# Optimization experiments

Hardware: AMD Instinct MI355X
Metric: run time of the kernel (lower is better)

## Reference

```python
import jax, jax.numpy as jnp
import numpy as np

B_, L_, D_MODEL, N_LAYER, VOCAB = 4, 2048, 512, 2, 128
D_INNER, D_STATE, DT_RANK, D_CONV = 2 * D_MODEL, 16, D_MODEL // 16, 4
NDIR = 2  # forward / backward Mamba stacks


def setup_inputs() -> dict:
    key = jax.random.key(0)
    ks = jax.random.split(key, 12)
    f = jax.random.normal
    A_init = jnp.broadcast_to(
        jnp.log(jnp.arange(1, D_STATE + 1, dtype=jnp.float32)),
        (NDIR, N_LAYER, D_INNER, D_STATE)) + 0.0
    return {
        "input_ids": jax.random.randint(ks[0], (B_, L_), 0, VOCAB),
        "padding_mask": jnp.ones((B_, L_), dtype=bool),
        "embed": 0.02 * f(ks[1], (NDIR, VOCAB, D_MODEL)),
        "in_proj_w": 0.02 * f(ks[2], (NDIR, N_LAYER, 2 * D_INNER, D_MODEL)),
        "conv_w": 0.1 * f(ks[3], (NDIR, N_LAYER, D_INNER, 1, D_CONV)),
        "conv_b": 0.1 * f(ks[4], (NDIR, N_LAYER, D_INNER)),
        "x_proj_w": 0.02 * f(ks[5], (NDIR, N_LAYER, DT_RANK + 2 * D_STATE, D_INNER)),
        "dt_proj_w": 0.1 * f(ks[6], (NDIR, N_LAYER, D_INNER, DT_RANK)),
        "dt_proj_b": -4.0 + 0.5 * jax.random.uniform(ks[7], (NDIR, N_LAYER, D_INNER)),
        "A_log": A_init,
        "D": jnp.ones((NDIR, N_LAYER, D_INNER)),
        "out_proj_w": 0.02 * f(ks[8], (NDIR, N_LAYER, D_MODEL, D_INNER)),
        "norm_w": jnp.ones((NDIR, N_LAYER, D_MODEL)),
        "norm_f_w": jnp.ones((NDIR, D_MODEL)),
        "proj_w": 0.02 * f(ks[9], (D_MODEL, 2 * D_MODEL)),
        "proj_b": jnp.zeros((D_MODEL,)),
    }


def _rmsnorm(x, w, eps=1e-5):
    return x * jax.lax.rsqrt(jnp.mean(jnp.square(x), axis=-1, keepdims=True) + eps) * w


def _selective_scan(u, dt, Bm, Cm, A, Dp):
    # u, dt: (b, l, d_inner); Bm, Cm: (b, l, d_state)
    b, l, di = u.shape

    def step(h, inp):
        u_t, dt_t, b_t, c_t = inp                      # (b,di) (b,di) (b,n) (b,n)
        dA = jnp.exp(dt_t[:, :, None] * A)             # (b, di, n)
        h = dA * h + (dt_t * u_t)[:, :, None] * b_t[:, None, :]
        return h, jnp.einsum('bdn,bn->bd', h, c_t)

    h0 = jnp.zeros((b, di, A.shape[-1]), u.dtype)
    xs = (jnp.swapaxes(u, 0, 1), jnp.swapaxes(dt, 0, 1),
          jnp.swapaxes(Bm, 0, 1), jnp.swapaxes(Cm, 0, 1))
    _, ys = jax.lax.scan(step, h0, xs)                 # ys: (l, b, di)
    return jnp.swapaxes(ys, 0, 1) + u * Dp


def _mamba(x, p):
    in_w, cw, cb, xw, dtw, dtb, alog, dp, ow = p
    xz = jnp.einsum('bld,ed->ble', x, in_w)            # (b, l, 2*d_inner)
    u, z = jnp.split(xz, 2, axis=-1)
    uc = jnp.swapaxes(u, 1, 2)                         # (b, d_inner, l)
    uc = jax.lax.conv_general_dilated(
        uc, cw, (1,), [(D_CONV - 1, 0)], feature_group_count=D_INNER)
    u = jax.nn.silu(jnp.swapaxes(uc + cb[None, :, None], 1, 2))
    xdbl = jnp.einsum('bld,ed->ble', u, xw)
    dt, Bm, Cm = jnp.split(xdbl, [DT_RANK, DT_RANK + D_STATE], axis=-1)
    dt = jax.nn.softplus(jnp.einsum('blr,dr->bld', dt, dtw) + dtb)
    y = _selective_scan(u, dt, Bm, Cm, -jnp.exp(alog), dp)
    y = y * jax.nn.silu(z)
    return jnp.einsum('bld,ed->ble', y, ow)


def _mixer(ids, d, embed, in_proj_w, conv_w, conv_b, x_proj_w, dt_proj_w,
           dt_proj_b, A_log, D, out_proj_w, norm_w, norm_f_w):
    hidden = embed[d][ids]
    residual = None
    for i in range(N_LAYER):
        residual = hidden if residual is None else hidden + residual
        hidden = _rmsnorm(residual, norm_w[d, i])
        p = (in_proj_w[d, i], conv_w[d, i], conv_b[d, i], x_proj_w[d, i],
             dt_proj_w[d, i], dt_proj_b[d, i], A_log[d, i], D[d, i],
             out_proj_w[d, i])
        hidden = _mamba(hidden, p)
    return _rmsnorm(hidden + residual, norm_f_w[d])


def reference(input_ids, padding_mask, embed, in_proj_w, conv_w, conv_b,
              x_proj_w, dt_proj_w, dt_proj_b, A_log, D, out_proj_w, norm_w,
              norm_f_w, proj_w, proj_b):
    args = (embed, in_proj_w, conv_w, conv_b, x_proj_w, dt_proj_w, dt_proj_b,
            A_log, D, out_proj_w, norm_w, norm_f_w)
    fwd = _mixer(input_ids, 0, *args)
    bwd = jnp.flip(_mixer(jnp.flip(input_ids, 1), 1, *args), 1)
    out = jnp.concatenate([fwd, bwd], axis=-1)        # (b, l, 2*d_model)
    return jnp.einsum('ble,oe->blo', out, proj_w) + proj_b
```

## Files before the change

kernel.cpp:

```cpp
#include <hip/hip_runtime.h>
#include <hip/hip_bf16.h>

#define B_   4
#define L_   2048
#define DM   512
#define DI   1024
#define NST  16
#define DTR  32
#define ROWS (B_ * L_)
#define NCHUNK 64
#define CLEN  (L_ / NCHUNK)
#define LN2R 1.4426950408889634f

typedef unsigned short u16;
typedef __attribute__((ext_vector_type(8))) short bf16x8;
typedef __attribute__((ext_vector_type(4))) float f32x4;
typedef __attribute__((ext_vector_type(4))) float float4v;
typedef __attribute__((ext_vector_type(2))) float f32x2;

__device__ __forceinline__ float bf2f(u16 h) {
  union { unsigned int u; float f; } v; v.u = ((unsigned int)h) << 16; return v.f;
}
__device__ __forceinline__ u16 f2bf(float f) {
  union { float f; unsigned int u; } v; v.f = f;
  unsigned int u = v.u;
  if ((u & 0x7fffffffu) > 0x7f800000u) return (u16)((u >> 16) | 0x0040u);
  return (u16)((u + 0x7fffu + ((u >> 16) & 1u)) >> 16);
}
__device__ __forceinline__ float sigmoidf_(float x) { return 1.f / (1.f + __expf(-x)); }

__device__ __forceinline__ f32x2 pk_mul(f32x2 a, f32x2 b) {
  f32x2 d; asm("v_pk_mul_f32 %0, %1, %2" : "=v"(d) : "v"(a), "v"(b)); return d;
}
__device__ __forceinline__ f32x2 pk_fma(f32x2 a, f32x2 b, f32x2 c) {
  f32x2 d; asm("v_pk_fma_f32 %0, %1, %2, %3" : "=v"(d) : "v"(a), "v"(b), "v"(c)); return d;
}

__device__ __forceinline__ void gload16(const u16* g, u16* l) {
  __builtin_amdgcn_global_load_lds(
      (const __attribute__((address_space(1))) void*)g,
      (__attribute__((address_space(3))) void*)l, 16, 0, 0);
}

__global__ __launch_bounds__(256) void cvt_k(const float* __restrict__ in,
                                             u16* __restrict__ out, int n4) {
  int i = blockIdx.x * 256 + threadIdx.x;
  if (i >= n4) return;
  float4v v = *(const float4v*)&in[i * 4];
  u16 o[4];
  o[0] = f2bf(v.x); o[1] = f2bf(v.y); o[2] = f2bf(v.z); o[3] = f2bf(v.w);
  *(ulong1*)&out[i * 4] = *(ulong1*)o;
}

__global__ __launch_bounds__(256) void trp_k(const float* __restrict__ in,
                                             float* __restrict__ out) {
  int o = blockIdx.x * 256 + threadIdx.x;
  int li = o >> 15;
  int k = (o >> 10) & (DTR - 1);
  int d = o & (DI - 1);
  out[o] = in[((size_t)li * DI + d) * DTR + k];
}

__global__ __launch_bounds__(256) void embed_k(const int* __restrict__ ids,
                                               const float* __restrict__ emb,
                                               float* __restrict__ res, int flip) {
  int idx = blockIdx.x * 256 + threadIdx.x;
  int c = idx & (DM - 1);
  int row = idx >> 9;
  int b = row >> 11;
  int l = row & (L_ - 1);
  int sl = flip ? (L_ - 1 - l) : l;
  int id = ids[(b << 11) + sl];
  res[idx] = emb[id * DM + c];
}

template <bool ADD>
__global__ __launch_bounds__(256) void addnorm_k(float* __restrict__ res,
                                                 const float* __restrict__ hid,
                                                 const float* __restrict__ w,
                                                 u16* __restrict__ xn) {
  int row = blockIdx.x;
  int tid = threadIdx.x;
  int base = row * DM;
  float x0 = res[base + tid];
  float x1 = res[base + 256 + tid];
  if (ADD) {
    x0 += hid[base + tid];
    x1 += hid[base + 256 + tid];
    res[base + tid] = x0;
    res[base + 256 + tid] = x1;
  }
  float s = x0 * x0 + x1 * x1;
  for (int off = 32; off; off >>= 1) s += __shfl_xor(s, off);
  __shared__ float ps[4];
  if (!(tid & 63)) ps[tid >> 6] = s;
  __syncthreads();
  float tot = ps[0] + ps[1] + ps[2] + ps[3];
  float rs = 1.f / sqrtf(tot / (float)DM + 1e-5f);
  xn[base + tid]       = f2bf(x0 * rs * w[tid]);
  xn[base + 256 + tid] = f2bf(x1 * rs * w[tid + 256]);
}

#define MFMA_B16(a, b, c) __builtin_amdgcn_mfma_f32_16x16x32_bf16(a, b, c, 0, 0, 0)

__global__ __launch_bounds__(512) void gemm8p_k(const u16* __restrict__ A,
                                                const u16* __restrict__ W,
                                                u16* __restrict__ outp,
                                                int N, int K) {
  __shared__ u16 As[2][2][256 * 32];
  __shared__ u16 Wsh[2][2][256 * 32];
  int tid = threadIdx.x;
  int lane = tid & 63;
  int wv = tid >> 6;
  int wr = wv >> 2, wc = wv & 3;
  int bid = blockIdx.x;
  int xcd = bid & 7, jj = bid >> 3;
  int mt = (xcd & 3) * 8 + (jj & 7);
  int nt = (xcd >> 2) * 4 + (jj >> 3);
  int m0 = mt * 256, n0 = nt * 256;
  f32x4 acc[8][4];
#pragma unroll
  for (int i = 0; i < 8; ++i)
#pragma unroll
    for (int j = 0; j < 4; ++j) acc[i][j] = (f32x4){0.f, 0.f, 0.f, 0.f};
  int rr = lane & 15;
  int sl = lane >> 4;
  int pofs = ((sl + (rr >> 1)) & 3) * 8;
  int lr = lane >> 2;
  int ls = ((lane & 3) - (lr >> 1)) & 3;

  auto stA = [&](int tau, int ks) {
    int buf = tau & 1;
#pragma unroll
    for (int j = 0; j < 2; ++j)
      gload16(A + (size_t)(m0 + j * 128 + wv * 16 + lr) * K + tau * 64 + ks * 32 + ls * 8,
              &As[buf][ks][(j * 128 + wv * 16) * 32]);
  };
  auto stW = [&](int tau, int ks) {
    int buf = tau & 1;
#pragma unroll
    for (int j = 0; j < 2; ++j)
      gload16(W + (size_t)(n0 + j * 128 + wv * 16 + lr) * K + tau * 64 + ks * 32 + ls * 8,
              &Wsh[buf][ks][(j * 128 + wv * 16) * 32]);
  };

  int NT = K / 64;
  stA(0, 0); stW(0, 0); stA(0, 1); stW(0, 1);
  asm volatile("s_waitcnt vmcnt(4)" ::: "memory");
  __builtin_amdgcn_sched_barrier(0);
  __builtin_amdgcn_s_barrier();
  __builtin_amdgcn_sched_barrier(0);

  for (int tau = 0; tau < NT; ++tau) {
    int buf = tau & 1;
    bool more = (tau + 1 < NT);
    bf16x8 af[8], w0, w1;
#pragma unroll
    for (int mi = 0; mi < 8; ++mi)
      af[mi] = *(bf16x8*)&As[buf][0][(wr * 128 + mi * 16 + rr) * 32 + pofs];
    w0 = *(bf16x8*)&Wsh[buf][0][(wc * 64 + 0 * 16 + rr) * 32 + pofs];
    w1 = *(bf16x8*)&Wsh[buf][0][(wc * 64 + 1 * 16 + rr) * 32 + pofs];
    if (more) stA(tau + 1, 0);
    __builtin_amdgcn_sched_barrier(0);
    __builtin_amdgcn_s_barrier();
    asm volatile("s_waitcnt lgkmcnt(0)" ::: "memory");
    __builtin_amdgcn_sched_barrier(0);
    __builtin_amdgcn_s_setprio(1);
#pragma unroll
    for (int mi = 0; mi < 8; ++mi) {
      acc[mi][0] = MFMA_B16(af[mi], w0, acc[mi][0]);
      acc[mi][1] = MFMA_B16(af[mi], w1, acc[mi][1]);
    }
    __builtin_amdgcn_s_setprio(0);
    __builtin_amdgcn_s_barrier();
    __builtin_amdgcn_sched_barrier(0);
    w0 = *(bf16x8*)&Wsh[buf][0][(wc * 64 + 2 * 16 + rr) * 32 + pofs];
    w1 = *(bf16x8*)&Wsh[buf][0][(wc * 64 + 3 * 16 + rr) * 32 + pofs];
    if (more) {
      stW(tau + 1, 0);
      asm volatile("s_waitcnt vmcnt(4)" ::: "memory");
    } else {
      asm volatile("s_waitcnt vmcnt(0)" ::: "memory");
    }
    __builtin_amdgcn_sched_barrier(0);
    __builtin_amdgcn_s_barrier();
    asm volatile("s_waitcnt lgkmcnt(0)" ::: "memory");
    __builtin_amdgcn_sched_barrier(0);
    __builtin_amdgcn_s_setprio(1);
#pragma unroll
    for (int mi = 0; mi < 8; ++mi) {
      acc[mi][2] = MFMA_B16(af[mi], w0, acc[mi][2]);
      acc[mi][3] = MFMA_B16(af[mi], w1, acc[mi][3]);
    }
    __builtin_amdgcn_s_setprio(0);
    __builtin_amdgcn_s_barrier();
    __builtin_amdgcn_sched_barrier(0);
#pragma unroll
    for (int mi = 0; mi < 8; ++mi)
      af[mi] = *(bf16x8*)&As[buf][1][(wr * 128 + mi * 16 + rr) * 32 + pofs];
    w0 = *(bf16x8*)&Wsh[buf][1][(wc * 64 + 0 * 16 + rr) * 32 + pofs];
    w1 = *(bf16x8*)&Wsh[buf][1][(wc * 64 + 1 * 16 + rr) * 32 + pofs];
    if (more) stA(tau + 1, 1);
    __builtin_amdgcn_sched_barrier(0);
    __builtin_amdgcn_s_barrier();
    asm volatile("s_waitcnt lgkmcnt(0)" ::: "memory");
    __builtin_amdgcn_sched_barrier(0);
    __builtin_amdgcn_s_setprio(1);
#pragma unroll
    for (int mi = 0; mi < 8; ++mi) {
      acc[mi][0] = MFMA_B16(af[mi], w0, acc[mi][0]);
      acc[mi][1] = MFMA_B16(af[mi], w1, acc[mi][1]);
    }
    __builtin_amdgcn_s_setprio(0);
    __builtin_amdgcn_s_barrier();
    __builtin_amdgcn_sched_barrier(0);
    w0 = *(bf16x8*)&Wsh[buf][1][(wc * 64 + 2 * 16 + rr) * 32 + pofs];
    w1 = *(bf16x8*)&Wsh[buf][1][(wc * 64 + 3 * 16 + rr) * 32 + pofs];
    if (more) {
      stW(tau + 1, 1);
      asm volatile("s_waitcnt vmcnt(4)" ::: "memory");
    }
    __builtin_amdgcn_sched_barrier(0);
    __builtin_amdgcn_s_barrier();
    asm volatile("s_waitcnt lgkmcnt(0)" ::: "memory");
    __builtin_amdgcn_sched_barrier(0);
    __builtin_amdgcn_s_setprio(1);
#pragma unroll
    for (int mi = 0; mi < 8; ++mi) {
      acc[mi][2] = MFMA_B16(af[mi], w0, acc[mi][2]);
      acc[mi][3] = MFMA_B16(af[mi], w1, acc[mi][3]);
    }
    __builtin_amdgcn_s_setprio(0);
    __builtin_amdgcn_s_barrier();
    __builtin_amdgcn_sched_barrier(0);
  }
  int cr = (lane >> 4) << 2;
  int cc = lane & 15;
#pragma unroll
  for (int mi = 0; mi < 8; ++mi)
#pragma unroll
    for (int ni = 0; ni < 4; ++ni) {
      int row = m0 + wr * 128 + mi * 16 + cr;
      int col = n0 + wc * 64 + ni * 16 + cc;
#pragma unroll
      for (int j = 0; j < 4; ++j)
        outp[(size_t)(row + j) * N + col] = f2bf(acc[mi][ni][j]);
    }
}

#define EPI_F32  0
#define EPI_BF16 1
#define EPI_BIAS 2

template <int BN, int EPI, int SK = 1>
__global__ __launch_bounds__(256) void gemm_bt(const u16* __restrict__ A,
                                               const u16* __restrict__ W,
                                               void* __restrict__ outp,
                                               const float* __restrict__ bias,
                                               int N, int K) {
  constexpr int BM = 128, BK = 32;
  constexpr int NF = BN / 32;
  constexpr int G = (BN == 128) ? 4 : 3;
  __shared__ u16 As[4][BM * BK];
  __shared__ u16 Wsh[4][BN * BK];
  int tid = threadIdx.x;
  int lane = tid & 63;
  int wv = tid >> 6;
  int wr = wv >> 1, wc = wv & 1;
  int m0 = blockIdx.x * BM;
  int n0 = (SK > 1) ? 0 : blockIdx.y * BN;
  int koff = (SK > 1) ? blockIdx.y * (K / SK) : 0;
  int KS = K / SK;
  int NK = KS / BK;
  f32x4 acc[4][NF];
#pragma unroll
  for (int i = 0; i < 4; ++i)
#pragma unroll
    for (int j = 0; j < NF; ++j) acc[i][j] = (f32x4){0.f, 0.f, 0.f, 0.f};
  int rr = lane & 15;
  int kk = (lane >> 4) << 3;
  int l4 = lane >> 2;
  int c8 = (lane & 3) << 3;
  const u16* Ag = A + (size_t)(m0 + l4) * K + koff + c8;
  const u16* Wg = W + (size_t)(n0 + l4) * K + koff + c8;

  auto stage = [&](int k0, int buf) {
    gload16(Ag + (size_t)(wv * 16) * K + k0, &As[buf][wv * 512]);
    gload16(Ag + (size_t)((wv + 4) * 16) * K + k0, &As[buf][(wv + 4) * 512]);
    gload16(Wg + (size_t)(wv * 16) * K + k0, &Wsh[buf][wv * 512]);
    if (BN == 128)
      gload16(Wg + (size_t)((wv + 4) * 16) * K + k0, &Wsh[buf][(wv + 4) * 512]);
  };

  stage(0, 0); stage(BK, 1); stage(2 * BK, 2);
  for (int k = 0; k < NK; ++k) {
    if (k < NK - 2)
      asm volatile("s_waitcnt vmcnt(%0)" :: "n"(2 * G) : "memory");
    else if (k == NK - 2)
      asm volatile("s_waitcnt vmcnt(%0)" :: "n"(G) : "memory");
    else
      asm volatile("s_waitcnt vmcnt(0)" ::: "memory");
    __builtin_amdgcn_s_barrier();
    __builtin_amdgcn_sched_barrier(0);
    if (k + 3 < NK) stage((k + 3) * BK, (k + 3) & 3);
    __builtin_amdgcn_sched_barrier(0);
    int cur = k & 3;
    bf16x8 af[4], wf[NF];
#pragma unroll
    for (int mi = 0; mi < 4; ++mi)
      af[mi] = *(bf16x8*)&As[cur][(wr * 64 + mi * 16 + rr) * BK + kk];
#pragma unroll
    for (int ni = 0; ni < NF; ++ni)
      wf[ni] = *(bf16x8*)&Wsh[cur][(wc * (BN / 2) + ni * 16 + rr) * BK + kk];
#pragma unroll
    for (int mi = 0; mi < 4; ++mi)
#pragma unroll
      for (int ni = 0; ni < NF; ++ni)
        acc[mi][ni] = __builtin_amdgcn_mfma_f32_16x16x32_bf16(af[mi], wf[ni], acc[mi][ni], 0, 0, 0);
  }
  int cr = (lane >> 4) << 2;
  int cc = lane & 15;
  float* outF = (float*)outp + ((SK > 1) ? (size_t)blockIdx.y * (size_t)ROWS * N : 0);
#pragma unroll
  for (int mi = 0; mi < 4; ++mi)
#pragma unroll
    for (int ni = 0; ni < NF; ++ni) {
      int row = m0 + wr * 64 + mi * 16 + cr;
      int col = n0 + wc * (BN / 2) + ni * 16 + cc;
      float bv = (EPI == EPI_BIAS) ? bias[col] : 0.f;
#pragma unroll
      for (int j = 0; j < 4; ++j) {
        float v = acc[mi][ni][j] + bv;
        if (EPI == EPI_BF16)
          ((u16*)outp)[(size_t)(row + j) * N + col] = f2bf(v);
        else
          outF[(size_t)(row + j) * N + col] = v;
      }
    }
}

__global__ __launch_bounds__(256) void conv_k(const u16* __restrict__ xz,
                                              const float* __restrict__ cw,
                                              const float* __restrict__ cb,
                                              u16* __restrict__ uh) {
  int idx = blockIdx.x * 256 + threadIdx.x;
  int c = idx & (DI - 1);
  int row = idx >> 10;
  int l = row & (L_ - 1);
  float acc = cb[c];
#pragma unroll
  for (int j = 0; j < 4; ++j) {
    int ls = l + j - 3;
    if (ls >= 0)
      acc += bf2f(xz[(size_t)(row + j - 3) * (2 * DI) + c]) * cw[c * 4 + j];
  }
  float s = acc * sigmoidf_(acc);
  uh[idx] = f2bf(s);
}

__device__ __forceinline__ bool a_fast(const float* alog, int d, float& a20) {
  a20 = -__expf(alog[d * NST]) * LN2R;
  bool fast = true;
#pragma unroll
  for (int n = 1; n < NST; ++n) {
    float an = -__expf(alog[d * NST + n]) * LN2R;
    fast &= (fabsf(an - (float)(n + 1) * a20) <= 1e-5f * (float)(n + 1) * fabsf(a20));
  }
  return fast;
}

__device__ __forceinline__ void stage_xs(float (*xs)[64], const float* xp,
                                         int b, int t0, int tid) {
  size_t base = ((size_t)b * L_ + t0) * 64;
  const float4v* s0 = (const float4v*)(xp + base);
  const float4v* s1 = (const float4v*)(xp + (size_t)ROWS * 64 + base);
  const float4v* s2 = (const float4v*)(xp + (size_t)2 * ROWS * 64 + base);
  const float4v* s3 = (const float4v*)(xp + (size_t)3 * ROWS * 64 + base);
  float4v* dst = (float4v*)&xs[0][0];
  dst[tid]       = s0[tid]       + s1[tid]       + s2[tid]       + s3[tid];
  dst[tid + 256] = s0[tid + 256] + s1[tid + 256] + s2[tid + 256] + s3[tid + 256];
}

__global__ __launch_bounds__(256) void dtscan1_k(const u16* __restrict__ uh,
                                                 const float* __restrict__ xp,
                                                 const float* __restrict__ dtw_t,
                                                 const float* __restrict__ dtb,
                                                 const float* __restrict__ alog,
                                                 float* __restrict__ dtf,
                                                 float* __restrict__ chk) {
  __shared__ float xs[CLEN][64];
  int blk = blockIdx.x;
  int db = blk & 3;
  int c  = (blk >> 2) & (NCHUNK - 1);
  int b  = blk >> 8;
  int tid = threadIdx.x;
  int d  = db * 256 + tid;
  int t0 = c * CLEN;
  stage_xs(xs, xp, b, t0, tid);
  f32x2 w2[16];
#pragma unroll
  for (int j = 0; j < 16; ++j)
    w2[j] = (f32x2){dtw_t[(size_t)(2 * j) * DI + d], dtw_t[(size_t)(2 * j + 1) * DI + d]};
  float bias = dtb[d];
  float a20;
  bool fast = a_fast(alog, d, a20);
  __syncthreads();
  float S = 0.f;
  size_t ubase = ((size_t)b * L_ + t0) * DI + d;
  f32x2 h2[8];
#pragma unroll
  for (int q = 0; q < 8; ++q) h2[q] = (f32x2){0.f, 0.f};
  for (int t = 0; t < CLEN; ++t) {
    f32x2 a2 = {bias, 0.f};
    const f32x2* xr2 = (const f32x2*)&xs[t][0];
#pragma unroll
    for (int j = 0; j < 16; ++j) a2 = pk_fma(xr2[j], w2[j], a2);
    float a = a2.x + a2.y;
    float dtv = (a > 15.f) ? a : __logf(1.f + __expf(a));
    dtf[ubase] = dtv;
    float du = dtv * bf2f(uh[ubase]);
    S += dtv;
    if (fast) {
      float p1 = exp2f(dtv * a20);
      float p2 = p1 * p1;
      f32x2 pw = {p1, p2};
      f32x2 pst = {p2, p2};
      f32x2 du2 = {du, du};
#pragma unroll
      for (int k = 0; k < 4; ++k) {
        f32x4 bv = *(const f32x4*)&xs[t][DTR + k * 4];
        f32x2 blo = __builtin_shufflevector(bv, bv, 0, 1);
        f32x2 bhi = __builtin_shufflevector(bv, bv, 2, 3);
        h2[2 * k]     = pk_fma(pw, h2[2 * k], pk_mul(du2, blo));
        pw = pk_mul(pw, pst);
        h2[2 * k + 1] = pk_fma(pw, h2[2 * k + 1], pk_mul(du2, bhi));
        if (k < 3) pw = pk_mul(pw, pst);
      }
    } else {
#pragma unroll
      for (int q = 0; q < 8; ++q) {
        float e0 = exp2f(dtv * -__expf(alog[d * NST + 2 * q]) * LN2R);
        float e1 = exp2f(dtv * -__expf(alog[d * NST + 2 * q + 1]) * LN2R);
        f32x2 bv = *(const f32x2*)&xs[t][DTR + q * 2];
        h2[q] = pk_fma((f32x2){e0, e1}, h2[q], pk_mul((f32x2){du, du}, bv));
      }
    }
    ubase += DI;
  }
  const size_t H = (size_t)B_ * NCHUNK * DI * NST;
  size_t idx = ((size_t)(b * NCHUNK + c) * DI + d) * NST;
#pragma unroll
  for (int n = 0; n < NST; ++n) {
    float an = -__expf(alog[d * NST + n]) * LN2R;
    chk[idx + n]     = exp2f(an * S);
    chk[H + idx + n] = (n & 1) ? h2[n >> 1].y : h2[n >> 1].x;
  }
}

__global__ __launch_bounds__(256) void scan2_k(float* __restrict__ chk) {
  int j = blockIdx.x * 256 + threadIdx.x;
  int n = j & 15;
  int d = (j >> 4) & (DI - 1);
  int b = j >> 14;
  const size_t H = (size_t)B_ * NCHUNK * DI * NST;
  float h = 0.f;
  for (int c = 0; c < NCHUNK; ++c) {
    size_t idx = ((size_t)(b * NCHUNK + c) * DI + d) * NST + n;
    float a = chk[idx];
    float hl = chk[H + idx];
    chk[H + idx] = h;
    h = a * h + hl;
  }
}

__global__ __launch_bounds__(256) void scan3_k(const u16* __restrict__ uh,
                                               const float* __restrict__ dtf,
                                               const float* __restrict__ xp,
                                               const float* __restrict__ alog,
                                               const float* __restrict__ dvec,
                                               const float* __restrict__ chk,
                                               const u16* __restrict__ xz,
                                               u16* __restrict__ yg) {
  __shared__ float xs[CLEN][64];
  int blk = blockIdx.x;
  int db = blk & 3;
  int c  = (blk >> 2) & (NCHUNK - 1);
  int b  = blk >> 8;
  int tid = threadIdx.x;
  int d  = db * 256 + tid;
  int t0 = c * CLEN;
  stage_xs(xs, xp, b, t0, tid);
  float a20;
  bool fast = a_fast(alog, d, a20);
  const size_t H = (size_t)B_ * NCHUNK * DI * NST;
  size_t cidx = ((size_t)(b * NCHUNK + c) * DI + d) * NST;
  f32x2 h2[8];
#pragma unroll
  for (int q = 0; q < 8; ++q) h2[q] = *(const f32x2*)&chk[H + cidx + 2 * q];
  float Dv = dvec[d];
  __syncthreads();
  size_t ubase = ((size_t)b * L_ + t0) * DI + d;
  size_t zbase = ((size_t)b * L_ + t0) * (2 * DI) + DI + d;
  if (fast) {
    for (int t = 0; t < CLEN; ++t) {
      float dtv = dtf[ubase];
      float uv  = bf2f(uh[ubase]);
      float du  = dtv * uv;
      float p1 = exp2f(dtv * a20);
      float p2 = p1 * p1;
      f32x2 pw = {p1, p2};
      f32x2 pst = {p2, p2};
      f32x2 du2 = {du, du};
      f32x2 acc2 = {0.f, 0.f};
#pragma unroll
      for (int k = 0; k < 4; ++k) {
        f32x4 bv = *(const f32x4*)&xs[t][DTR + k * 4];
        f32x4 cv = *(const f32x4*)&xs[t][DTR + NST + k * 4];
        f32x2 blo = __builtin_shufflevector(bv, bv, 0, 1);
        f32x2 bhi = __builtin_shufflevector(bv, bv, 2, 3);
        f32x2 clo = __builtin_shufflevector(cv, cv, 0, 1);
        f32x2 chi = __builtin_shufflevector(cv, cv, 2, 3);
        h2[2 * k]     = pk_fma(pw, h2[2 * k], pk_mul(du2, blo));
        acc2          = pk_fma(h2[2 * k], clo, acc2);
        pw = pk_mul(pw, pst);
        h2[2 * k + 1] = pk_fma(pw, h2[2 * k + 1], pk_mul(du2, bhi));
        acc2          = pk_fma(h2[2 * k + 1], chi, acc2);
        if (k < 3) pw = pk_mul(pw, pst);
      }
      float y = acc2.x + acc2.y + uv * Dv;
      float z = bf2f(xz[zbase]);
      yg[ubase] = f2bf(y * z * sigmoidf_(z));
      ubase += DI; zbase += 2 * DI;
    }
  } else {
    float A2[NST];
#pragma unroll
    for (int n = 0; n < NST; ++n) A2[n] = -__expf(alog[d * NST + n]) * LN2R;
    for (int t = 0; t < CLEN; ++t) {
      float dtv = dtf[ubase];
      float uv  = bf2f(uh[ubase]);
      float du  = dtv * uv;
      f32x2 acc2 = {0.f, 0.f};
#pragma unroll
      for (int q = 0; q < 8; ++q) {
        f32x2 bv = *(const f32x2*)&xs[t][DTR + q * 2];
        f32x2 cv = *(const f32x2*)&xs[t][DTR + NST + q * 2];
        f32x2 e = {exp2f(dtv * A2[2 * q]), exp2f(dtv * A2[2 * q + 1])};
        h2[q] = pk_fma(e, h2[q], pk_mul((f32x2){du, du}, bv));
        acc2 = pk_fma(h2[q], cv, acc2);
      }
      float y = acc2.x + acc2.y + uv * Dv;
      float z = bf2f(xz[zbase]);
      yg[ubase] = f2bf(y * z * sigmoidf_(z));
      ubase += DI; zbase += 2 * DI;
    }
  }
}

__global__ __launch_bounds__(256) void fincat_k(const float* __restrict__ hid,
                                                const float* __restrict__ res,
                                                const float* __restrict__ w,
                                                u16* __restrict__ cat, int dir) {
  int row = blockIdx.x;
  int tid = threadIdx.x;
  int base = row * DM;
  float x0 = hid[base + tid] + res[base + tid];
  float x1 = hid[base + 256 + tid] + res[base + 256 + tid];
  float s = x0 * x0 + x1 * x1;
  for (int off = 32; off; off >>= 1) s += __shfl_xor(s, off);
  __shared__ float ps[4];
  if (!(tid & 63)) ps[tid >> 6] = s;
  __syncthreads();
  float tot = ps[0] + ps[1] + ps[2] + ps[3];
  float rs = 1.f / sqrtf(tot / (float)DM + 1e-5f);
  int b = row >> 11, l = row & (L_ - 1);
  size_t drow = dir ? ((size_t)(b << 11) + (L_ - 1 - l)) : (size_t)row;
  size_t obase = drow * (2 * DM) + (size_t)dir * DM;
  cat[obase + tid]       = f2bf(x0 * rs * w[tid]);
  cat[obase + 256 + tid] = f2bf(x1 * rs * w[tid + 256]);
}

extern "C" void kernel_launch(void* const* d_in, const int* in_sizes, int n_in,
                              void* d_out, int out_size, void* d_ws, size_t ws_size,
                              hipStream_t stream) {
  const int*   ids      = (const int*)d_in[0];
  const float* embed    = (const float*)d_in[2];
  const float* in_w     = (const float*)d_in[3];
  const float* conv_w   = (const float*)d_in[4];
  const float* conv_b   = (const float*)d_in[5];
  const float* x_w      = (const float*)d_in[6];
  const float* dt_w     = (const float*)d_in[7];
  const float* dt_bias  = (const float*)d_in[8];
  const float* A_log    = (const float*)d_in[9];
  const float* Dp       = (const float*)d_in[10];
  const float* out_w    = (const float*)d_in[11];
  const float* norm_w   = (const float*)d_in[12];
  const float* norm_f   = (const float*)d_in[13];
  const float* proj_w   = (const float*)d_in[14];
  const float* proj_b   = (const float*)d_in[15];

  char* ws = (char*)d_ws;
  size_t off = 0;
  auto alloc = [&](size_t bytes) {
    void* p = ws + off;
    off += (bytes + 255) & ~(size_t)255;
    return p;
  };
  float* res  = (float*)alloc((size_t)ROWS * DM * 4);
  float* hid  = (float*)alloc((size_t)ROWS * DM * 4);
  u16*   xnyg = (u16*)alloc((size_t)ROWS * DI * 2);
  u16*   xz   = (u16*)alloc((size_t)ROWS * 2 * DI * 2);
  u16*   u_h  = (u16*)alloc((size_t)ROWS * DI * 2);
  float* dtf  = (float*)alloc((size_t)ROWS * DI * 4);
  float* chk  = (float*)alloc((size_t)2 * B_ * NCHUNK * DI * NST * 4);
  u16*   cat  = (u16*)alloc((size_t)ROWS * 2 * DM * 2);
  const int N_IN  = 4 * 2 * DI * DM;
  const int N_XW  = 4 * 64 * DI;
  const int N_OW  = 4 * DM * DI;
  const int N_PW  = DM * 2 * DM;
  const int N_DTW = 4 * DTR * DI;
  u16*   in_wb  = (u16*)alloc((size_t)N_IN * 2);
  u16*   x_wb   = (u16*)alloc((size_t)N_XW * 2);
  u16*   out_wb = (u16*)alloc((size_t)N_OW * 2);
  u16*   pr_wb  = (u16*)alloc((size_t)N_PW * 2);
  float* dtw_t  = (float*)alloc((size_t)N_DTW * 4);
  if (off > ws_size) return;

  cvt_k<<<(N_IN / 4 + 255) / 256, 256, 0, stream>>>(in_w, in_wb, N_IN / 4);
  cvt_k<<<(N_XW / 4 + 255) / 256, 256, 0, stream>>>(x_w, x_wb, N_XW / 4);
  cvt_k<<<(N_OW / 4 + 255) / 256, 256, 0, stream>>>(out_w, out_wb, N_OW / 4);
  cvt_k<<<(N_PW / 4 + 255) / 256, 256, 0, stream>>>(proj_w, pr_wb, N_PW / 4);
  trp_k<<<N_DTW / 256, 256, 0, stream>>>(dt_w, dtw_t);

  for (int d = 0; d < 2; ++d) {
    embed_k<<<ROWS * DM / 256, 256, 0, stream>>>(ids, embed + (size_t)d * 128 * DM, res, d);
    for (int i = 0; i < 2; ++i) {
      int li = d * 2 + i;
      if (i == 0)
        addnorm_k<false><<<ROWS, 256, 0, stream>>>(res, hid, norm_w + (size_t)li * DM, xnyg);
      else
        addnorm_k<true><<<ROWS, 256, 0, stream>>>(res, hid, norm_w + (size_t)li * DM, xnyg);
      gemm8p_k<<<256, 512, 0, stream>>>(
          xnyg, in_wb + (size_t)li * 2 * DI * DM, xz, 2 * DI, DM);
      conv_k<<<ROWS * DI / 256, 256, 0, stream>>>(
          xz, conv_w + (size_t)li * DI * 4, conv_b + (size_t)li * DI, u_h);
      gemm_bt<64, EPI_F32, 4><<<dim3(ROWS / 128, 4), 256, 0, stream>>>(
          u_h, x_wb + (size_t)li * 64 * DI, hid, nullptr, 64, DI);
      dtscan1_k<<<B_ * NCHUNK * (DI / 256), 256, 0, stream>>>(
          u_h, hid, dtw_t + (size_t)li * DTR * DI, dt_bias + (size_t)li * DI,
          A_log + (size_t)li * DI * NST, dtf, chk);
      scan2_k<<<(B_ * DI * NST) / 256, 256, 0, stream>>>(chk);
      scan3_k<<<B_ * NCHUNK * (DI / 256), 256, 0, stream>>>(
          u_h, dtf, hid, A_log + (size_t)li * DI * NST, Dp + (size_t)li * DI, chk,
          xz, xnyg);
      gemm_bt<64, EPI_F32><<<dim3(ROWS / 128, DM / 64), 256, 0, stream>>>(
          xnyg, out_wb + (size_t)li * DM * DI, hid, nullptr, DM, DI);
    }
    fincat_k<<<ROWS, 256, 0, stream>>>(hid, res, norm_f + (size_t)d * DM, cat, d);
  }
  gemm_bt<64, EPI_BIAS><<<dim3(ROWS / 128, DM / 64), 256, 0, stream>>>(
      cat, pr_wb, (float*)d_out, proj_b, DM, DI);
}
```

Baseline: 823.3 us.

## Batch both Mamba directions into shared launches and recompute dt in the scan

Both direction stacks now run as one doubled batch of 16384 rows. Each kernel derives its direction from the row or block index and picks per-direction weights from that, which halves the kernel launches and gives the GEMMs and scans larger grids. The dt buffer is removed: scan3 recomputes dt from the x_proj output and the dt weights instead of reading a float array. The scan chunk count drops from 64 to 32 per sequence, the in-proj output is split into separate u and z buffers, and the chunk-state, u and concat buffers share one aliased workspace region. In exchange, the dt dot product is computed twice, and longer chunks mean more serial work per scan block.

```diff
diff --git a/kernel.cpp b/kernel.cpp
--- a/kernel.cpp
+++ b/kernel.cpp
@@ -7,8 +7,9 @@
 #define DI   1024
 #define NST  16
 #define DTR  32
-#define ROWS (B_ * L_)
-#define NCHUNK 64
+#define ROWS  (B_ * L_)
+#define ROWS2 (2 * ROWS)
+#define NCHUNK 32
 #define CLEN  (L_ / NCHUNK)
 #define LN2R 1.4426950408889634f
 
@@ -63,23 +64,28 @@
 
 __global__ __launch_bounds__(256) void embed_k(const int* __restrict__ ids,
                                                const float* __restrict__ emb,
-                                               float* __restrict__ res, int flip) {
+                                               float* __restrict__ res) {
   int idx = blockIdx.x * 256 + threadIdx.x;
   int c = idx & (DM - 1);
   int row = idx >> 9;
-  int b = row >> 11;
-  int l = row & (L_ - 1);
-  int sl = flip ? (L_ - 1 - l) : l;
+  int dir = row >> 13;
+  int r = row & (ROWS - 1);
+  int b = r >> 11;
+  int l = r & (L_ - 1);
+  int sl = dir ? (L_ - 1 - l) : l;
   int id = ids[(b << 11) + sl];
-  res[idx] = emb[id * DM + c];
+  res[idx] = emb[(size_t)dir * 128 * DM + id * DM + c];
 }
 
 template <bool ADD>
 __global__ __launch_bounds__(256) void addnorm_k(float* __restrict__ res,
                                                  const float* __restrict__ hid,
-                                                 const float* __restrict__ w,
+                                                 const float* __restrict__ norm_w,
+                                                 int layer,
                                                  u16* __restrict__ xn) {
   int row = blockIdx.x;
+  int dir = row >> 13;
+  const float* w = norm_w + (size_t)(dir * 2 + layer) * DM;
   int tid = threadIdx.x;
   int base = row * DM;
   float x0 = res[base + tid];
@@ -105,8 +111,9 @@
 
 __global__ __launch_bounds__(512) void gemm8p_k(const u16* __restrict__ A,
                                                 const u16* __restrict__ W,
-                                                u16* __restrict__ outp,
-                                                int N, int K) {
+                                                u16* __restrict__ outU,
+                                                u16* __restrict__ outZ,
+                                                int K) {
   __shared__ u16 As[2][2][256 * 32];
   __shared__ u16 Wsh[2][2][256 * 32];
   int tid = threadIdx.x;
@@ -115,9 +122,10 @@
   int wr = wv >> 2, wc = wv & 3;
   int bid = blockIdx.x;
   int xcd = bid & 7, jj = bid >> 3;
-  int mt = (xcd & 3) * 8 + (jj & 7);
-  int nt = (xcd >> 2) * 4 + (jj >> 3);
+  int mt = xcd * 8 + (jj & 7);
+  int nt = jj >> 3;
   int m0 = mt * 256, n0 = nt * 256;
+  const u16* Weff = W + (size_t)(m0 >> 13) * (size_t)2 * (2 * DI) * DM;
   f32x4 acc[8][4];
 #pragma unroll
   for (int i = 0; i < 8; ++i)
@@ -140,7 +148,7 @@
     int buf = tau & 1;
 #pragma unroll
     for (int j = 0; j < 2; ++j)
-      gload16(W + (size_t)(n0 + j * 128 + wv * 16 + lr) * K + tau * 64 + ks * 32 + ls * 8,
+      gload16(Weff + (size_t)(n0 + j * 128 + wv * 16 + lr) * K + tau * 64 + ks * 32 + ls * 8,
               &Wsh[buf][ks][(j * 128 + wv * 16) * 32]);
   };
 
@@ -236,15 +244,17 @@
   }
   int cr = (lane >> 4) << 2;
   int cc = lane & 15;
+  u16* outp = (n0 < DI) ? outU : outZ;
+  int cb0 = (n0 < DI) ? n0 : (n0 - DI);
 #pragma unroll
   for (int mi = 0; mi < 8; ++mi)
 #pragma unroll
     for (int ni = 0; ni < 4; ++ni) {
       int row = m0 + wr * 128 + mi * 16 + cr;
-      int col = n0 + wc * 64 + ni * 16 + cc;
+      int col = cb0 + wc * 64 + ni * 16 + cc;
 #pragma unroll
       for (int j = 0; j < 4; ++j)
-        outp[(size_t)(row + j) * N + col] = f2bf(acc[mi][ni][j]);
+        outp[(size_t)(row + j) * DI + col] = f2bf(acc[mi][ni][j]);
     }
 }
 
@@ -257,7 +267,7 @@
                                                const u16* __restrict__ W,
                                                void* __restrict__ outp,
                                                const float* __restrict__ bias,
-                                               int N, int K) {
+                                               int N, int K, size_t wsd) {
   constexpr int BM = 128, BK = 32;
   constexpr int NF = BN / 32;
   constexpr int G = (BN == 128) ? 4 : 3;
@@ -272,6 +282,7 @@
   int koff = (SK > 1) ? blockIdx.y * (K / SK) : 0;
   int KS = K / SK;
   int NK = KS / BK;
+  const u16* Weff = W + (size_t)(m0 >> 13) * wsd;
   f32x4 acc[4][NF];
 #pragma unroll
   for (int i = 0; i < 4; ++i)
@@ -282,7 +293,7 @@
   int l4 = lane >> 2;
   int c8 = (lane & 3) << 3;
   const u16* Ag = A + (size_t)(m0 + l4) * K + koff + c8;
-  const u16* Wg = W + (size_t)(n0 + l4) * K + koff + c8;
+  const u16* Wg = Weff + (size_t)(n0 + l4) * K + koff + c8;
 
   auto stage = [&](int k0, int buf) {
     gload16(Ag + (size_t)(wv * 16) * K + k0, &As[buf][wv * 512]);
@@ -320,7 +331,8 @@
   }
   int cr = (lane >> 4) << 2;
   int cc = lane & 15;
-  float* outF = (float*)outp + ((SK > 1) ? (size_t)blockIdx.y * (size_t)ROWS * N : 0);
+  float* outF = (float*)outp +
+      ((SK > 1) ? (size_t)blockIdx.y * (size_t)gridDim.x * BM * N : 0);
 #pragma unroll
   for (int mi = 0; mi < 4; ++mi)
 #pragma unroll
@@ -339,20 +351,24 @@
     }
 }
 
-__global__ __launch_bounds__(256) void conv_k(const u16* __restrict__ xz,
-                                              const float* __restrict__ cw,
-                                              const float* __restrict__ cb,
+__global__ __launch_bounds__(256) void conv_k(const u16* __restrict__ xzu,
+                                              const float* __restrict__ conv_w,
+                                              const float* __restrict__ conv_b,
+                                              int layer,
                                               u16* __restrict__ uh) {
   int idx = blockIdx.x * 256 + threadIdx.x;
   int c = idx & (DI - 1);
   int row = idx >> 10;
+  int dir = row >> 13;
   int l = row & (L_ - 1);
+  const float* cw = conv_w + (size_t)(dir * 2 + layer) * DI * 4;
+  const float* cb = conv_b + (size_t)(dir * 2 + layer) * DI;
   float acc = cb[c];
 #pragma unroll
   for (int j = 0; j < 4; ++j) {
     int ls = l + j - 3;
     if (ls >= 0)
-      acc += bf2f(xz[(size_t)(row + j - 3) * (2 * DI) + c]) * cw[c * 4 + j];
+      acc += bf2f(xzu[(size_t)(row + j - 3) * DI + c]) * cw[c * 4 + j];
   }
   float s = acc * sigmoidf_(acc);
   uh[idx] = f2bf(s);
@@ -370,54 +386,65 @@
 }
 
 __device__ __forceinline__ void stage_xs(float (*xs)[64], const float* xp,
-                                         int b, int t0, int tid) {
-  size_t base = ((size_t)b * L_ + t0) * 64;
+                                         size_t rowbase, int tid) {
+  size_t base = rowbase * 64;
   const float4v* s0 = (const float4v*)(xp + base);
-  const float4v* s1 = (const float4v*)(xp + (size_t)ROWS * 64 + base);
-  const float4v* s2 = (const float4v*)(xp + (size_t)2 * ROWS * 64 + base);
-  const float4v* s3 = (const float4v*)(xp + (size_t)3 * ROWS * 64 + base);
+  const float4v* s1 = (const float4v*)(xp + (size_t)ROWS2 * 64 + base);
+  const float4v* s2 = (const float4v*)(xp + (size_t)2 * ROWS2 * 64 + base);
+  const float4v* s3 = (const float4v*)(xp + (size_t)3 * ROWS2 * 64 + base);
   float4v* dst = (float4v*)&xs[0][0];
-  dst[tid]       = s0[tid]       + s1[tid]       + s2[tid]       + s3[tid];
-  dst[tid + 256] = s0[tid + 256] + s1[tid + 256] + s2[tid + 256] + s3[tid + 256];
+#pragma unroll
+  for (int i = 0; i < CLEN / 16; ++i)
+    dst[tid + i * 256] = s0[tid + i * 256] + s1[tid + i * 256] +
+                         s2[tid + i * 256] + s3[tid + i * 256];
+}
+
+__device__ __forceinline__ float dt_of(const float (*xs)[64], int t,
+                                       const f32x2* w2, float bias) {
+  f32x2 a2 = {bias, 0.f};
+  const f32x2* xr2 = (const f32x2*)&xs[t][0];
+#pragma unroll
+  for (int j = 0; j < 16; ++j) a2 = pk_fma(xr2[j], w2[j], a2);
+  float a = a2.x + a2.y;
+  return (a > 15.f) ? a : __logf(1.f + __expf(a));
 }
 
 __global__ __launch_bounds__(256) void dtscan1_k(const u16* __restrict__ uh,
                                                  const float* __restrict__ xp,
                                                  const float* __restrict__ dtw_t,
                                                  const float* __restrict__ dtb,
-                                                 const float* __restrict__ alog,
-                                                 float* __restrict__ dtf,
+                                                 const float* __restrict__ alog_,
+                                                 int layer,
                                                  float* __restrict__ chk) {
   __shared__ float xs[CLEN][64];
   int blk = blockIdx.x;
   int db = blk & 3;
   int c  = (blk >> 2) & (NCHUNK - 1);
-  int b  = blk >> 8;
+  int nb = blk >> 7;
+  int dir = nb >> 2;
   int tid = threadIdx.x;
   int d  = db * 256 + tid;
+  int li = dir * 2 + layer;
+  const float* dtwT = dtw_t + (size_t)li * DTR * DI;
+  const float* alog = alog_ + (size_t)li * DI * NST;
   int t0 = c * CLEN;
-  stage_xs(xs, xp, b, t0, tid);
+  size_t rowbase = (size_t)nb * L_ + t0;
+  stage_xs(xs, xp, rowbase, tid);
   f32x2 w2[16];
 #pragma unroll
   for (int j = 0; j < 16; ++j)
-    w2[j] = (f32x2){dtw_t[(size_t)(2 * j) * DI + d], dtw_t[(size_t)(2 * j + 1) * DI + d]};
-  float bias = dtb[d];
+    w2[j] = (f32x2){dtwT[(size_t)(2 * j) * DI + d], dtwT[(size_t)(2 * j + 1) * DI + d]};
+  float bias = dtb[(size_t)li * DI + d];
   float a20;
   bool fast = a_fast(alog, d, a20);
   __syncthreads();
   float S = 0.f;
-  size_t ubase = ((size_t)b * L_ + t0) * DI + d;
+  size_t ubase = rowbase * DI + d;
   f32x2 h2[8];
 #pragma unroll
   for (int q = 0; q < 8; ++q) h2[q] = (f32x2){0.f, 0.f};
   for (int t = 0; t < CLEN; ++t) {
-    f32x2 a2 = {bias, 0.f};
-    const f32x2* xr2 = (const f32x2*)&xs[t][0];
-#pragma unroll
-    for (int j = 0; j < 16; ++j) a2 = pk_fma(xr2[j], w2[j], a2);
-    float a = a2.x + a2.y;
-    float dtv = (a > 15.f) ? a : __logf(1.f + __expf(a));
-    dtf[ubase] = dtv;
+    float dtv = dt_of(xs, t, w2, bias);
     float du = dtv * bf2f(uh[ubase]);
     S += dtv;
     if (fast) {
@@ -447,8 +474,8 @@
     }
     ubase += DI;
   }
-  const size_t H = (size_t)B_ * NCHUNK * DI * NST;
-  size_t idx = ((size_t)(b * NCHUNK + c) * DI + d) * NST;
+  const size_t H = (size_t)8 * NCHUNK * DI * NST;
+  size_t idx = ((size_t)(nb * NCHUNK + c) * DI + d) * NST;
 #pragma unroll
   for (int n = 0; n < NST; ++n) {
     float an = -__expf(alog[d * NST + n]) * LN2R;
@@ -461,11 +488,11 @@
   int j = blockIdx.x * 256 + threadIdx.x;
   int n = j & 15;
   int d = (j >> 4) & (DI - 1);
-  int b = j >> 14;
-  const size_t H = (size_t)B_ * NCHUNK * DI * NST;
+  int nb = j >> 14;
+  const size_t H = (size_t)8 * NCHUNK * DI * NST;
   float h = 0.f;
   for (int c = 0; c < NCHUNK; ++c) {
-    size_t idx = ((size_t)(b * NCHUNK + c) * DI + d) * NST + n;
+    size_t idx = ((size_t)(nb * NCHUNK + c) * DI + d) * NST + n;
     float a = chk[idx];
     float hl = chk[H + idx];
     chk[H + idx] = h;
@@ -474,36 +501,47 @@
 }
 
 __global__ __launch_bounds__(256) void scan3_k(const u16* __restrict__ uh,
-                                               const float* __restrict__ dtf,
                                                const float* __restrict__ xp,
-                                               const float* __restrict__ alog,
-                                               const float* __restrict__ dvec,
+                                               const float* __restrict__ dtw_t,
+                                               const float* __restrict__ dtb,
+                                               const float* __restrict__ alog_,
+                                               const float* __restrict__ Dp,
+                                               int layer,
                                                const float* __restrict__ chk,
-                                               const u16* __restrict__ xz,
+                                               const u16* __restrict__ xzz,
                                                u16* __restrict__ yg) {
   __shared__ float xs[CLEN][64];
   int blk = blockIdx.x;
   int db = blk & 3;
   int c  = (blk >> 2) & (NCHUNK - 1);
-  int b  = blk >> 8;
+  int nb = blk >> 7;
+  int dir = nb >> 2;
   int tid = threadIdx.x;
   int d  = db * 256 + tid;
+  int li = dir * 2 + layer;
+  const float* dtwT = dtw_t + (size_t)li * DTR * DI;
+  const float* alog = alog_ + (size_t)li * DI * NST;
   int t0 = c * CLEN;
-  stage_xs(xs, xp, b, t0, tid);
+  size_t rowbase = (size_t)nb * L_ + t0;
+  stage_xs(xs, xp, rowbase, tid);
+  f32x2 w2[16];
+#pragma unroll
+  for (int j = 0; j < 16; ++j)
+    w2[j] = (f32x2){dtwT[(size_t)(2 * j) * DI + d], dtwT[(size_t)(2 * j + 1) * DI + d]};
+  float bias = dtb[(size_t)li * DI + d];
   float a20;
   bool fast = a_fast(alog, d, a20);
-  const size_t H = (size_t)B_ * NCHUNK * DI * NST;
-  size_t cidx = ((size_t)(b * NCHUNK + c) * DI + d) * NST;
+  const size_t H = (size_t)8 * NCHUNK * DI * NST;
+  size_t cidx = ((size_t)(nb * NCHUNK + c) * DI + d) * NST;
   f32x2 h2[8];
 #pragma unroll
   for (int q = 0; q < 8; ++q) h2[q] = *(const f32x2*)&chk[H + cidx + 2 * q];
-  float Dv = dvec[d];
+  float Dv = Dp[(size_t)li * DI + d];
   __syncthreads();
-  size_t ubase = ((size_t)b * L_ + t0) * DI + d;
-  size_t zbase = ((size_t)b * L_ + t0) * (2 * DI) + DI + d;
+  size_t ubase = rowbase * DI + d;
   if (fast) {
     for (int t = 0; t < CLEN; ++t) {
-      float dtv = dtf[ubase];
+      float dtv = dt_of(xs, t, w2, bias);
       float uv  = bf2f(uh[ubase]);
       float du  = dtv * uv;
       float p1 = exp2f(dtv * a20);
@@ -528,16 +566,16 @@
         if (k < 3) pw = pk_mul(pw, pst);
       }
       float y = acc2.x + acc2.y + uv * Dv;
-      float z = bf2f(xz[zbase]);
+      float z = bf2f(xzz[ubase]);
       yg[ubase] = f2bf(y * z * sigmoidf_(z));
-      ubase += DI; zbase += 2 * DI;
+      ubase += DI;
     }
   } else {
     float A2[NST];
 #pragma unroll
     for (int n = 0; n < NST; ++n) A2[n] = -__expf(alog[d * NST + n]) * LN2R;
     for (int t = 0; t < CLEN; ++t) {
-      float dtv = dtf[ubase];
+      float dtv = dt_of(xs, t, w2, bias);
       float uv  = bf2f(uh[ubase]);
       float du  = dtv * uv;
       f32x2 acc2 = {0.f, 0.f};
@@ -550,18 +588,20 @@
         acc2 = pk_fma(h2[q], cv, acc2);
       }
       float y = acc2.x + acc2.y + uv * Dv;
-      float z = bf2f(xz[zbase]);
+      float z = bf2f(xzz[ubase]);
       yg[ubase] = f2bf(y * z * sigmoidf_(z));
-      ubase += DI; zbase += 2 * DI;
+      ubase += DI;
     }
   }
 }
 
 __global__ __launch_bounds__(256) void fincat_k(const float* __restrict__ hid,
                                                 const float* __restrict__ res,
-                                                const float* __restrict__ w,
-                                                u16* __restrict__ cat, int dir) {
+                                                const float* __restrict__ norm_f,
+                                                u16* __restrict__ cat) {
   int row = blockIdx.x;
+  int dir = row >> 13;
+  const float* w = norm_f + (size_t)dir * DM;
   int tid = threadIdx.x;
   int base = row * DM;
   float x0 = hid[base + tid] + res[base + tid];
@@ -573,8 +613,9 @@
   __syncthreads();
   float tot = ps[0] + ps[1] + ps[2] + ps[3];
   float rs = 1.f / sqrtf(tot / (float)DM + 1e-5f);
-  int b = row >> 11, l = row & (L_ - 1);
-  size_t drow = dir ? ((size_t)(b << 11) + (L_ - 1 - l)) : (size_t)row;
+  int r = row & (ROWS - 1);
+  int b = r >> 11, l = r & (L_ - 1);
+  size_t drow = dir ? ((size_t)(b << 11) + (L_ - 1 - l)) : (size_t)r;
   size_t obase = drow * (2 * DM) + (size_t)dir * DM;
   cat[obase + tid]       = f2bf(x0 * rs * w[tid]);
   cat[obase + 256 + tid] = f2bf(x1 * rs * w[tid + 256]);
@@ -606,14 +647,12 @@
     off += (bytes + 255) & ~(size_t)255;
     return p;
   };
-  float* res  = (float*)alloc((size_t)ROWS * DM * 4);
-  float* hid  = (float*)alloc((size_t)ROWS * DM * 4);
-  u16*   xnyg = (u16*)alloc((size_t)ROWS * DI * 2);
-  u16*   xz   = (u16*)alloc((size_t)ROWS * 2 * DI * 2);
-  u16*   u_h  = (u16*)alloc((size_t)ROWS * DI * 2);
-  float* dtf  = (float*)alloc((size_t)ROWS * DI * 4);
-  float* chk  = (float*)alloc((size_t)2 * B_ * NCHUNK * DI * NST * 4);
-  u16*   cat  = (u16*)alloc((size_t)ROWS * 2 * DM * 2);
+  float* res  = (float*)alloc((size_t)ROWS2 * DM * 4);
+  float* hid  = (float*)alloc((size_t)ROWS2 * DM * 4);
+  u16*   xnyg = (u16*)alloc((size_t)ROWS2 * DI * 2);
+  u16*   xzz  = (u16*)alloc((size_t)ROWS2 * DI * 2);
+  void*  shrd = alloc((size_t)ROWS2 * DI * 2);
+  u16*   u_h  = (u16*)alloc((size_t)ROWS2 * DI * 2);
   const int N_IN  = 4 * 2 * DI * DM;
   const int N_XW  = 4 * 64 * DI;
   const int N_OW  = 4 * DM * DI;
@@ -626,38 +665,35 @@
   float* dtw_t  = (float*)alloc((size_t)N_DTW * 4);
   if (off > ws_size) return;
 
+  u16*   xzu = (u16*)shrd;
+  float* chk = (float*)shrd;
+  u16*   cat = (u16*)shrd;
+
   cvt_k<<<(N_IN / 4 + 255) / 256, 256, 0, stream>>>(in_w, in_wb, N_IN / 4);
   cvt_k<<<(N_XW / 4 + 255) / 256, 256, 0, stream>>>(x_w, x_wb, N_XW / 4);
   cvt_k<<<(N_OW / 4 + 255) / 256, 256, 0, stream>>>(out_w, out_wb, N_OW / 4);
   cvt_k<<<(N_PW / 4 + 255) / 256, 256, 0, stream>>>(proj_w, pr_wb, N_PW / 4);
   trp_k<<<N_DTW / 256, 256, 0, stream>>>(dt_w, dtw_t);
 
-  for (int d = 0; d < 2; ++d) {
-    embed_k<<<ROWS * DM / 256, 256, 0, stream>>>(ids, embed + (size_t)d * 128 * DM, res, d);
-    for (int i = 0; i < 2; ++i) {
-      int li = d * 2 + i;
-      if (i == 0)
-        addnorm_k<false><<<ROWS, 256, 0, stream>>>(res, hid, norm_w + (size_t)li * DM, xnyg);
-      else
-        addnorm_k<true><<<ROWS, 256, 0, stream>>>(res, hid, norm_w + (size_t)li * DM, xnyg);
-      gemm8p_k<<<256, 512, 0, stream>>>(
-          xnyg, in_wb + (size_t)li * 2 * DI * DM, xz, 2 * DI, DM);
-      conv_k<<<ROWS * DI / 256, 256, 0, stream>>>(
-          xz, conv_w + (size_t)li * DI * 4, conv_b + (size_t)li * DI, u_h);
-      gemm_bt<64, EPI_F32, 4><<<dim3(ROWS / 128, 4), 256, 0, stream>>>(
-          u_h, x_wb + (size_t)li * 64 * DI, hid, nullptr, 64, DI);
-      dtscan1_k<<<B_ * NCHUNK * (DI / 256), 256, 0, stream>>>(
-          u_h, hid, dtw_t + (size_t)li * DTR * DI, dt_bias + (size_t)li * DI,
-          A_log + (size_t)li * DI * NST, dtf, chk);
-      scan2_k<<<(B_ * DI * NST) / 256, 256, 0, stream>>>(chk);
-      scan3_k<<<B_ * NCHUNK * (DI / 256), 256, 0, stream>>>(
-          u_h, dtf, hid, A_log + (size_t)li * DI * NST, Dp + (size_t)li * DI, chk,
-          xz, xnyg);
-      gemm_bt<64, EPI_F32><<<dim3(ROWS / 128, DM / 64), 256, 0, stream>>>(
-          xnyg, out_wb + (size_t)li * DM * DI, hid, nullptr, DM, DI);
-    }
-    fincat_k<<<ROWS, 256, 0, stream>>>(hid, res, norm_f + (size_t)d * DM, cat, d);
-  }
+  embed_k<<<ROWS2 * DM / 256, 256, 0, stream>>>(ids, embed, res);
+  for (int i = 0; i < 2; ++i) {
+    if (i == 0)
+      addnorm_k<false><<<ROWS2, 256, 0, stream>>>(res, hid, norm_w, i, xnyg);
+    else
+      addnorm_k<true><<<ROWS2, 256, 0, stream>>>(res, hid, norm_w, i, xnyg);
+    gemm8p_k<<<512, 512, 0, stream>>>(
+        xnyg, in_wb + (size_t)i * 2 * DI * DM, xzu, xzz, DM);
+    conv_k<<<ROWS2 * DI / 256, 256, 0, stream>>>(xzu, conv_w, conv_b, i, u_h);
+    gemm_bt<64, EPI_F32, 4><<<dim3(ROWS2 / 128, 4), 256, 0, stream>>>(
+        u_h, x_wb + (size_t)i * 64 * DI, hid, nullptr, 64, DI, (size_t)2 * 64 * DI);
+    dtscan1_k<<<1024, 256, 0, stream>>>(u_h, hid, dtw_t, dt_bias, A_log, i, chk);
+    scan2_k<<<512, 256, 0, stream>>>(chk);
+    scan3_k<<<1024, 256, 0, stream>>>(u_h, hid, dtw_t, dt_bias, A_log, Dp, i,
+                                      chk, xzz, xnyg);
+    gemm_bt<64, EPI_F32><<<dim3(ROWS2 / 128, DM / 64), 256, 0, stream>>>(
+        xnyg, out_wb + (size_t)i * DM * DI, hid, nullptr, DM, DI, (size_t)2 * DM * DI);
+  }
+  fincat_k<<<ROWS2, 256, 0, stream>>>(hid, res, norm_f, cat);
   gemm_bt<64, EPI_BIAS><<<dim3(ROWS / 128, DM / 64), 256, 0, stream>>>(
-      cat, pr_wb, (float*)d_out, proj_b, DM, DI);
-}
+      cat, pr_wb, (float*)d_out, proj_b, DM, DI, 0);
+}
```

After: 775.3 us. 5.8% less time.
